# Kernel tuning notes

Measured on AMD Instinct MI355X. Metric: run time of the kernel, lower is better.

## Reference

```python
import jax, jax.numpy as jnp
import numpy as np

TEMPERATURE = 0.07


def _unit(k, shape):
    x = jax.random.normal(k, shape, dtype=jnp.float32)
    return x / jnp.linalg.norm(x, axis=-1, keepdims=True)


def setup_inputs() -> dict:
    key = jax.random.key(0)
    ks = jax.random.split(key, 7)
    B, Cml, Cmc, D = 8192, 2048, 1000, 512
    features = _unit(ks[0], (B, D))
    ml_text = _unit(ks[1], (Cml, D))
    mc_text = _unit(ks[2], (Cmc, D))
    multilabel_targets = (jax.random.uniform(ks[3], (B, Cml)) < 0.05).astype(jnp.float32)
    # one-hot multiclass targets
    mc_idx = jax.random.randint(ks[4], (B,), 0, Cmc)
    multiclass_targets = jax.nn.one_hot(mc_idx, Cmc, dtype=jnp.float32)
    dataset_indices = jax.random.randint(ks[5], (B,), 0, 2).astype(jnp.int32)
    ratios = jax.random.uniform(ks[6], (Cml,), minval=0.05, maxval=0.95, dtype=jnp.float32)
    return {
        "features": features,
        "multilabel_text_features": ml_text,
        "multiclass_text_features": mc_text,
        "multilabel_targets": multilabel_targets,
        "multiclass_targets": multiclass_targets,
        "dataset_indices": dataset_indices,
        "ratios": ratios,
    }


def iterate_M(sim_matrix, b, num_iterations=2):
    # sim_matrix: [B, C, 2]; b: [C, 2]
    P = jnp.exp(sim_matrix)
    for _ in range(num_iterations):
        P = P / P.sum(axis=2, keepdims=True)          # row (last-dim) normalize
        P = P / (P.sum(axis=0) / b)                   # column normalize to marginals b
    return P


def iterate_P(sim_matrix, m, num_iterations=5):
    # sim_matrix: [B, C]
    P = jnp.exp(sim_matrix)
    for _ in range(num_iterations):
        row_sums = P.sum(axis=1)
        P = P / jnp.maximum(row_sums, 1.0)[:, None]
        P = P * m / P.sum()
    return P


def reference(features, multilabel_text_features, multiclass_text_features,
              multilabel_targets, multiclass_targets, dataset_indices, ratios):
    ml_sim = features @ multilabel_text_features.T / TEMPERATURE   # [B, Cml]
    mc_sim = features @ multiclass_text_features.T / TEMPERATURE   # [B, Cmc]

    n_mc = jnp.sum(dataset_indices == 1).astype(jnp.float32)
    n_ml = jnp.sum(dataset_indices == 0).astype(jnp.float32)
    m = n_mc + n_ml * 0.1

    P = iterate_P(mc_sim, m, 5)

    bs = ml_sim.shape[0]
    sim3 = jnp.stack([ml_sim / 2, -ml_sim / 2], axis=-1)           # [B, Cml, 2]
    b = jnp.stack([ratios, 1.0 - ratios], axis=1) * bs             # [Cml, 2]
    M = iterate_M(sim3, b, 2)

    ml_targets_final = jnp.stack([multilabel_targets, 1.0 - multilabel_targets], axis=-1)
    multilabel_loss = -jnp.sum(ml_targets_final * jnp.log(M)) * 0.5
    multiclass_loss = -jnp.sum(multiclass_targets * jnp.log(P))
    total_loss = multiclass_loss + multilabel_loss
    return total_loss
```

## Files before the change

### kernel.cpp

```cpp
#include <hip/hip_runtime.h>

typedef unsigned short u16;
typedef float f32x4 __attribute__((ext_vector_type(4)));
typedef short s16x8 __attribute__((ext_vector_type(8)));

#define GPTR(x) ((const __attribute__((address_space(1))) void*)(x))
#define LPTR(x) ((__attribute__((address_space(3))) void*)(x))

__device__ __forceinline__ u16 f32_to_bf16(float f) {
  unsigned u = __builtin_bit_cast(unsigned, f);
  u += 0x7FFFu + ((u >> 16) & 1u);
  return (u16)(u >> 16);
}
__device__ __forceinline__ float bf16_to_f32(u16 h) {
  unsigned u = ((unsigned)h) << 16;
  return __builtin_bit_cast(float, u);
}

__global__ void k_cvt4(const float* __restrict__ in, u16* __restrict__ out, int n4) {
  int i = blockIdx.x * 256 + threadIdx.x;
  if (i >= n4) return;
  float4 v = reinterpret_cast<const float4*>(in)[i];
  ushort4 o;
  o.x = f32_to_bf16(v.x); o.y = f32_to_bf16(v.y);
  o.z = f32_to_bf16(v.z); o.w = f32_to_bf16(v.w);
  reinterpret_cast<ushort4*>(out)[i] = o;
}

__global__ void k_cvt_pad4(const float* __restrict__ in, u16* __restrict__ out, int nreal_rows) {
  int i = blockIdx.x * 256 + threadIdx.x;
  if (i >= 1024 * 128) return;
  int row = (i * 4) >> 9;
  ushort4 o = {0, 0, 0, 0};
  if (row < nreal_rows) {
    float4 v = reinterpret_cast<const float4*>(in)[i];
    o.x = f32_to_bf16(v.x); o.y = f32_to_bf16(v.y);
    o.z = f32_to_bf16(v.z); o.w = f32_to_bf16(v.w);
  }
  reinterpret_cast<ushort4*>(out)[i] = o;
}

template <bool COLSUM>
__global__ __launch_bounds__(256) void k_gemm_bt(
    const u16* __restrict__ A, const u16* __restrict__ B,
    u16* __restrict__ Cbf, float* __restrict__ colpart, int N, float scale)
{
  constexpr int K = 512;
  constexpr int BK = 64;
  __shared__ __align__(16) u16 As[128 * BK];
  __shared__ __align__(16) u16 Bs[128 * BK];
  const int tid  = threadIdx.x;
  const int lane = tid & 63;
  const int wave = tid >> 6;
  const int wr = wave >> 1, wc = wave & 1;
  const int row0 = blockIdx.x * 128;
  const int col0 = blockIdx.y * 128;

  f32x4 acc[4][4];
#pragma unroll
  for (int i = 0; i < 4; ++i)
#pragma unroll
    for (int j = 0; j < 4; ++j) acc[i][j] = (f32x4){0.f, 0.f, 0.f, 0.f};

  for (int k0 = 0; k0 < K; k0 += BK) {
    __syncthreads();
#pragma unroll
    for (int q = 0; q < 4; ++q) {
      int base = wave * 256 + q * 64;
      int slot = base + lane;
      int r = slot >> 3, s = slot & 7;
      int sg = s ^ (r & 7);
      __builtin_amdgcn_global_load_lds(GPTR(A + (size_t)(row0 + r) * K + k0 + sg * 8),
                                       LPTR(&As[base * 8]), 16, 0, 0);
      __builtin_amdgcn_global_load_lds(GPTR(B + (size_t)(col0 + r) * K + k0 + sg * 8),
                                       LPTR(&Bs[base * 8]), 16, 0, 0);
    }
    __syncthreads();
#pragma unroll
    for (int ks = 0; ks < 2; ++ks) {
      s16x8 af[4], bf[4];
#pragma unroll
      for (int mm = 0; mm < 4; ++mm) {
        int r = wr * 64 + mm * 16 + (lane & 15);
        int ss = (ks * 4 + (lane >> 4)) ^ (r & 7);
        af[mm] = *reinterpret_cast<const s16x8*>(&As[r * BK + ss * 8]);
      }
#pragma unroll
      for (int nn = 0; nn < 4; ++nn) {
        int r = wc * 64 + nn * 16 + (lane & 15);
        int ss = (ks * 4 + (lane >> 4)) ^ (r & 7);
        bf[nn] = *reinterpret_cast<const s16x8*>(&Bs[r * BK + ss * 8]);
      }
#pragma unroll
      for (int mm = 0; mm < 4; ++mm)
#pragma unroll
        for (int nn = 0; nn < 4; ++nn)
          acc[mm][nn] = __builtin_amdgcn_mfma_f32_16x16x32_bf16(af[mm], bf[nn], acc[mm][nn], 0, 0, 0);
    }
  }
  const int cr = (lane >> 4) * 4;
  const int cc = lane & 15;
#pragma unroll
  for (int mm = 0; mm < 4; ++mm) {
    int orow = row0 + wr * 64 + mm * 16 + cr;
#pragma unroll
    for (int nn = 0; nn < 4; ++nn) {
      int ocol = col0 + wc * 64 + nn * 16 + cc;
#pragma unroll
      for (int r = 0; r < 4; ++r)
        Cbf[(size_t)(orow + r) * N + ocol] = f32_to_bf16(acc[mm][nn][r] * scale);
    }
  }

  if constexpr (COLSUM) {
    __shared__ float cp[128];
    if (tid < 128) cp[tid] = 0.f;
    __syncthreads();
#pragma unroll
    for (int nn = 0; nn < 4; ++nn) {
      float cs = 0.f;
#pragma unroll
      for (int mm = 0; mm < 4; ++mm)
#pragma unroll
        for (int r = 0; r < 4; ++r) {
          float s = acc[mm][nn][r] * scale;
          cs += 1.f / (1.f + __expf(-s));
        }
      cs += __shfl_xor(cs, 16);
      cs += __shfl_xor(cs, 32);
      if (lane < 16) atomicAdd(&cp[wc * 64 + nn * 16 + lane], cs);
    }
    __syncthreads();
    if (tid < 128) colpart[(size_t)blockIdx.x * 2048 + col0 + tid] = cp[tid];
  }
}

__global__ void k_reduce_c(const float* __restrict__ part, const float* __restrict__ ratios,
                           float* __restrict__ c) {
  int j = blockIdx.x * 256 + threadIdx.x;
  float s = 0.f;
  for (int ch = 0; ch < 64; ++ch) s += part[ch * 2048 + j];
  float b0 = ratios[j] * 8192.f;
  float b1 = (1.f - ratios[j]) * 8192.f;
  c[2 * j]     = b0 / s;
  c[2 * j + 1] = b1 / (8192.f - s);
}

__global__ __launch_bounds__(256) void k_ml_pass2(
    const u16* __restrict__ S, const float* __restrict__ T, const float* __restrict__ c,
    float* __restrict__ part2, float* __restrict__ partT, float* __restrict__ partE)
{
  const int t = threadIdx.x;
  const int r0 = blockIdx.x * 8;
  float c0[8], c1[8];
#pragma unroll
  for (int q = 0; q < 4; ++q) {
    float4 cv = reinterpret_cast<const float4*>(c)[t * 4 + q];
    c0[q * 2]     = cv.x; c1[q * 2]     = cv.y;
    c0[q * 2 + 1] = cv.z; c1[q * 2 + 1] = cv.w;
  }

  float q0s[8], ts[8];
#pragma unroll
  for (int k = 0; k < 8; ++k) { q0s[k] = 0.f; ts[k] = 0.f; }
  float tss = 0.f, ldsum = 0.f;

#pragma unroll 2
  for (int r = 0; r < 8; ++r) {
    size_t row = r0 + r;
    s16x8 sv = *reinterpret_cast<const s16x8*>(S + row * 2048 + t * 8);
    float4 ta = reinterpret_cast<const float4*>(T + row * 2048)[t * 2];
    float4 tb = reinterpret_cast<const float4*>(T + row * 2048)[t * 2 + 1];
    float tv[8] = {ta.x, ta.y, ta.z, ta.w, tb.x, tb.y, tb.z, tb.w};
#pragma unroll
    for (int k = 0; k < 8; ++k) {
      float s = bf16_to_f32((u16)sv[k]);
      float e = __expf(s);
      float n0 = e * c0[k];
      float den = n0 + c1[k];
      q0s[k] += n0 * __builtin_amdgcn_rcpf(den);
      ldsum  += __logf(den);
      ts[k]  += tv[k];
      tss    += tv[k] * s;
    }
  }
  float es = tss - ldsum;
#pragma unroll
  for (int k = 0; k < 8; ++k)
    es += __logf(c0[k] / c1[k]) * ts[k] + 8.f * __logf(c1[k]);

  float* p2 = part2 + (size_t)blockIdx.x * 2048 + t * 8;
  float* pT = partT + (size_t)blockIdx.x * 2048 + t * 8;
#pragma unroll
  for (int q = 0; q < 2; ++q) {
    reinterpret_cast<float4*>(p2)[q] = (float4){q0s[q*4], q0s[q*4+1], q0s[q*4+2], q0s[q*4+3]};
    reinterpret_cast<float4*>(pT)[q] = (float4){ts[q*4], ts[q*4+1], ts[q*4+2], ts[q*4+3]};
  }

  __shared__ float red[256];
  red[t] = es;
  __syncthreads();
  for (int o = 128; o; o >>= 1) {
    if (t < o) red[t] += red[t + o];
    __syncthreads();
  }
  if (t == 0) partE[blockIdx.x] = red[0];
}

__global__ __launch_bounds__(256) void k_colredA(
    const float* __restrict__ part2, const float* __restrict__ partT,
    float* __restrict__ pA2, float* __restrict__ pAT)
{
  int j = blockIdx.x * 256 + threadIdx.x;
  int ch0 = blockIdx.y * 128;
  float cs2 = 0.f, Tj = 0.f;
  for (int ch = ch0; ch < ch0 + 128; ++ch) {
    cs2 += part2[(size_t)ch * 2048 + j];
    Tj  += partT[(size_t)ch * 2048 + j];
  }
  pA2[(size_t)blockIdx.y * 2048 + j] = cs2;
  pAT[(size_t)blockIdx.y * 2048 + j] = Tj;
}

__global__ __launch_bounds__(256) void k_colredB(
    const float* __restrict__ pA2, const float* __restrict__ pAT,
    const float* __restrict__ ratios, float* __restrict__ partCol)
{
  int j = blockIdx.x * 256 + threadIdx.x;
  float cs2 = 0.f, Tj = 0.f;
  for (int ch = 0; ch < 8; ++ch) {
    cs2 += pA2[(size_t)ch * 2048 + j];
    Tj  += pAT[(size_t)ch * 2048 + j];
  }
  float b0 = ratios[j] * 8192.f;
  float b1 = (1.f - ratios[j]) * 8192.f;
  float colp = Tj * __logf(b0 / cs2) + (8192.f - Tj) * __logf(b1 / (8192.f - cs2));
  __shared__ float red[256];
  red[threadIdx.x] = colp;
  __syncthreads();
  for (int o = 128; o; o >>= 1) {
    if (threadIdx.x < o) red[threadIdx.x] += red[threadIdx.x + o];
    __syncthreads();
  }
  if (threadIdx.x == 0) partCol[blockIdx.x] = red[0];
}

__global__ __launch_bounds__(256) void k_mc_rows(
    const u16* __restrict__ S2, const float* __restrict__ T2,
    float* __restrict__ R, float* __restrict__ rowdot, float* __restrict__ trow)
{
  int wave = threadIdx.x >> 6, lane = threadIdx.x & 63;
  int row = blockIdx.x * 4 + wave;
  const u16* s = S2 + (size_t)row * 1024;
  const float* t = T2 + (size_t)row * 1000;
  float re = 0.f, rd = 0.f, tr = 0.f;
#pragma unroll
  for (int g0 = 0; g0 < 2; ++g0) {
    int g = lane + g0 * 64;
    if (g < 125) {
      s16x8 sv = *reinterpret_cast<const s16x8*>(s + g * 8);
      float4 ta = reinterpret_cast<const float4*>(t)[g * 2];
      float4 tb = reinterpret_cast<const float4*>(t)[g * 2 + 1];
      float tv[8] = {ta.x, ta.y, ta.z, ta.w, tb.x, tb.y, tb.z, tb.w};
#pragma unroll
      for (int k = 0; k < 8; ++k) {
        float sf = bf16_to_f32((u16)sv[k]);
        re += __expf(sf);
        rd += tv[k] * sf;
        tr += tv[k];
      }
    }
  }
#pragma unroll
  for (int o = 32; o; o >>= 1) {
    re += __shfl_down(re, o);
    rd += __shfl_down(rd, o);
    tr += __shfl_down(tr, o);
  }
  if (lane == 0) { R[row] = re; rowdot[row] = rd; trow[row] = tr; }
}

__global__ __launch_bounds__(1024) void k_finalize(
    const float* __restrict__ R, const float* __restrict__ rowdot, const float* __restrict__ trow,
    const int* __restrict__ ds,
    const float* __restrict__ partE, const float* __restrict__ partCol,
    float* __restrict__ out)
{
  __shared__ float red[1024];
  const int tid = threadIdx.x;

  auto bsum = [&](float v) -> float {
    __syncthreads();
    red[tid] = v;
    __syncthreads();
    for (int o = 512; o; o >>= 1) {
      if (tid < o) red[tid] += red[tid + o];
      __syncthreads();
    }
    return red[0];
  };

  float nmc = 0.f, nml = 0.f;
  for (int i = tid; i < 8192; i += 1024) {
    int d = ds[i];
    nmc += (d == 1) ? 1.f : 0.f;
    nml += (d == 0) ? 1.f : 0.f;
  }
  float n_mc = bsum(nmc);
  float n_ml = bsum(nml);
  float m = n_mc + 0.1f * n_ml;

  float a[8], Rv[8];
#pragma unroll
  for (int q = 0; q < 8; ++q) { Rv[q] = R[tid + q * 1024]; a[q] = 1.f; }
  for (int it = 0; it < 5; ++it) {
    float p = 0.f;
#pragma unroll
    for (int q = 0; q < 8; ++q) {
      a[q] = a[q] / fmaxf(Rv[q] * a[q], 1.f);
      p += Rv[q] * a[q];
    }
    float tot = bsum(p);
    float sc = m / tot;
#pragma unroll
    for (int q = 0; q < 8; ++q) a[q] *= sc;
  }
  float mcp = 0.f;
#pragma unroll
  for (int q = 0; q < 8; ++q) {
    int i = tid + q * 1024;
    mcp += rowdot[i] + trow[i] * __logf(a[q]);
  }

  float ep = partE[tid];
  float cp = 0.f;
  if (tid < 8) cp = partCol[tid];

  float total = bsum(-mcp - 0.5f * (cp + ep));
  if (tid == 0) out[0] = total;
}

extern "C" void kernel_launch(void* const* d_in, const int* in_sizes, int n_in,
                              void* d_out, int out_size, void* d_ws, size_t ws_size,
                              hipStream_t stream)
{
  const float* features = (const float*)d_in[0];
  const float* ml_text  = (const float*)d_in[1];
  const float* mc_text  = (const float*)d_in[2];
  const float* ml_tgt   = (const float*)d_in[3];
  const float* mc_tgt   = (const float*)d_in[4];
  const int*   dsidx    = (const int*)d_in[5];
  const float* ratios   = (const float*)d_in[6];
  float* out = (float*)d_out;

  char* ws = (char*)d_ws;
  size_t off = 0;
  auto alloc = [&](size_t bytes) -> void* {
    void* p = ws + off;
    off += (bytes + 255) & ~(size_t)255;
    return p;
  };
  u16*   Abf    = (u16*)alloc((size_t)8192 * 512 * 2);
  u16*   MLbf   = (u16*)alloc((size_t)2048 * 512 * 2);
  u16*   MCbf   = (u16*)alloc((size_t)1024 * 512 * 2);
  u16*   Sml    = (u16*)alloc((size_t)8192 * 2048 * 2);
  u16*   Smc    = (u16*)alloc((size_t)8192 * 1024 * 2);
  float* part1  = (float*)alloc((size_t)64 * 2048 * 4);
  float* cbuf   = (float*)alloc((size_t)2048 * 2 * 4);
  float* part2  = (float*)alloc((size_t)1024 * 2048 * 4);
  float* partT  = (float*)alloc((size_t)1024 * 2048 * 4);
  float* pA2    = (float*)alloc((size_t)8 * 2048 * 4);
  float* pAT    = (float*)alloc((size_t)8 * 2048 * 4);
  float* partE  = (float*)alloc((size_t)1024 * 4);
  float* partCol= (float*)alloc((size_t)8 * 4);
  float* Rbuf   = (float*)alloc((size_t)8192 * 4);
  float* rdot   = (float*)alloc((size_t)8192 * 4);
  float* trow   = (float*)alloc((size_t)8192 * 4);

  k_cvt4<<<(8192 * 128 + 255) / 256, 256, 0, stream>>>(features, Abf, 8192 * 128);
  k_cvt4<<<(2048 * 128 + 255) / 256, 256, 0, stream>>>(ml_text, MLbf, 2048 * 128);
  k_cvt_pad4<<<(1024 * 128 + 255) / 256, 256, 0, stream>>>(mc_text, MCbf, 1000);

  const float scale = 1.0f / 0.07f;
  k_gemm_bt<true ><<<dim3(64, 16), 256, 0, stream>>>(Abf, MLbf, Sml, part1, 2048, scale);
  k_gemm_bt<false><<<dim3(64, 8),  256, 0, stream>>>(Abf, MCbf, Smc, nullptr, 1024, scale);

  k_reduce_c<<<8, 256, 0, stream>>>(part1, ratios, cbuf);
  k_ml_pass2<<<1024, 256, 0, stream>>>(Sml, ml_tgt, cbuf, part2, partT, partE);
  k_mc_rows<<<2048, 256, 0, stream>>>(Smc, mc_tgt, Rbuf, rdot, trow);
  k_colredA<<<dim3(8, 8), 256, 0, stream>>>(part2, partT, pA2, pAT);
  k_colredB<<<8, 256, 0, stream>>>(pA2, pAT, ratios, partCol);
  k_finalize<<<1, 1024, 0, stream>>>(Rbuf, rdot, trow, dsidx, partE, partCol, out);
}
```

Measured before the change: 130.7 us.

## Fuse multiclass row reductions into GEMM epilogue and merge conversion kernels

Result: slower. 143.4 us (+9.7%).

```diff
diff --git a/kernel.cpp b/kernel.cpp
--- a/kernel.cpp
+++ b/kernel.cpp
@@ -17,33 +17,35 @@
   return __builtin_bit_cast(float, u);
 }
 
-__global__ void k_cvt4(const float* __restrict__ in, u16* __restrict__ out, int n4) {
+__global__ __launch_bounds__(256) void k_cvt_all(
+    const float* __restrict__ A, const float* __restrict__ ML, const float* __restrict__ MC,
+    u16* __restrict__ Abf, u16* __restrict__ MLbf, u16* __restrict__ MCbf)
+{
   int i = blockIdx.x * 256 + threadIdx.x;
-  if (i >= n4) return;
-  float4 v = reinterpret_cast<const float4*>(in)[i];
-  ushort4 o;
-  o.x = f32_to_bf16(v.x); o.y = f32_to_bf16(v.y);
-  o.z = f32_to_bf16(v.z); o.w = f32_to_bf16(v.w);
-  reinterpret_cast<ushort4*>(out)[i] = o;
-}
-
-__global__ void k_cvt_pad4(const float* __restrict__ in, u16* __restrict__ out, int nreal_rows) {
-  int i = blockIdx.x * 256 + threadIdx.x;
-  if (i >= 1024 * 128) return;
-  int row = (i * 4) >> 9;
+  const float* src; u16* dst; int idx;
+  bool pad = false;
+  if (i < 1048576) { src = A; dst = Abf; idx = i; }
+  else if (i < 1310720) { src = ML; dst = MLbf; idx = i - 1048576; }
+  else if (i < 1441792) {
+    idx = i - 1310720; src = MC; dst = MCbf;
+    pad = ((idx * 4) >> 9) >= 1000;
+  } else return;
   ushort4 o = {0, 0, 0, 0};
-  if (row < nreal_rows) {
-    float4 v = reinterpret_cast<const float4*>(in)[i];
+  if (!pad) {
+    float4 v = reinterpret_cast<const float4*>(src)[idx];
     o.x = f32_to_bf16(v.x); o.y = f32_to_bf16(v.y);
     o.z = f32_to_bf16(v.z); o.w = f32_to_bf16(v.w);
   }
-  reinterpret_cast<ushort4*>(out)[i] = o;
-}
-
-template <bool COLSUM>
+  reinterpret_cast<ushort4*>(dst)[idx] = o;
+}
+
+template <int MODE>
 __global__ __launch_bounds__(256) void k_gemm_bt(
     const u16* __restrict__ A, const u16* __restrict__ B,
-    u16* __restrict__ Cbf, float* __restrict__ colpart, int N, float scale)
+    u16* __restrict__ Cbf, float* __restrict__ colpart,
+    const float* __restrict__ T2, float* __restrict__ pexp,
+    float* __restrict__ prdt, float* __restrict__ ptrw,
+    int N, float scale)
 {
   constexpr int K = 512;
   constexpr int BK = 64;
@@ -55,6 +57,8 @@
   const int wr = wave >> 1, wc = wave & 1;
   const int row0 = blockIdx.x * 128;
   const int col0 = blockIdx.y * 128;
+  const int cr = (lane >> 4) * 4;
+  const int cc = lane & 15;
 
   f32x4 acc[4][4];
 #pragma unroll
@@ -98,21 +102,19 @@
           acc[mm][nn] = __builtin_amdgcn_mfma_f32_16x16x32_bf16(af[mm], bf[nn], acc[mm][nn], 0, 0, 0);
     }
   }
-  const int cr = (lane >> 4) * 4;
-  const int cc = lane & 15;
-#pragma unroll
-  for (int mm = 0; mm < 4; ++mm) {
-    int orow = row0 + wr * 64 + mm * 16 + cr;
-#pragma unroll
-    for (int nn = 0; nn < 4; ++nn) {
-      int ocol = col0 + wc * 64 + nn * 16 + cc;
-#pragma unroll
-      for (int r = 0; r < 4; ++r)
-        Cbf[(size_t)(orow + r) * N + ocol] = f32_to_bf16(acc[mm][nn][r] * scale);
-    }
-  }
-
-  if constexpr (COLSUM) {
+
+  if constexpr (MODE == 0) {
+#pragma unroll
+    for (int mm = 0; mm < 4; ++mm) {
+      int orow = row0 + wr * 64 + mm * 16 + cr;
+#pragma unroll
+      for (int nn = 0; nn < 4; ++nn) {
+        int ocol = col0 + wc * 64 + nn * 16 + cc;
+#pragma unroll
+        for (int r = 0; r < 4; ++r)
+          Cbf[(size_t)(orow + r) * N + ocol] = f32_to_bf16(acc[mm][nn][r] * scale);
+      }
+    }
     __shared__ float cp[128];
     if (tid < 128) cp[tid] = 0.f;
     __syncthreads();
@@ -132,6 +134,56 @@
     }
     __syncthreads();
     if (tid < 128) colpart[(size_t)blockIdx.x * 2048 + col0 + tid] = cp[tid];
+  }
+
+  if constexpr (MODE == 1) {
+    float ex[16], rd[16], tw[16];
+#pragma unroll
+    for (int mm = 0; mm < 4; ++mm)
+#pragma unroll
+      for (int r = 0; r < 4; ++r) {
+        float e = 0.f, d = 0.f, w = 0.f;
+        int row = row0 + wr * 64 + mm * 16 + cr + r;
+#pragma unroll
+        for (int nn = 0; nn < 4; ++nn) {
+          int ocol = col0 + wc * 64 + nn * 16 + cc;
+          float s = acc[mm][nn][r] * scale;
+          if (ocol < 1000) {
+            float t = T2[(size_t)row * 1000 + ocol];
+            e += __expf(s);
+            d += t * s;
+            w += t;
+          }
+        }
+        ex[mm * 4 + r] = e; rd[mm * 4 + r] = d; tw[mm * 4 + r] = w;
+      }
+#pragma unroll
+    for (int o = 1; o < 16; o <<= 1)
+#pragma unroll
+      for (int q = 0; q < 16; ++q) {
+        ex[q] += __shfl_xor(ex[q], o);
+        rd[q] += __shfl_xor(rd[q], o);
+        tw[q] += __shfl_xor(tw[q], o);
+      }
+    __shared__ float rex[128][2], rrd[128][2], rtw[128][2];
+    if ((lane & 15) == 0) {
+#pragma unroll
+      for (int mm = 0; mm < 4; ++mm)
+#pragma unroll
+        for (int r = 0; r < 4; ++r) {
+          int lrow = wr * 64 + mm * 16 + cr + r;
+          rex[lrow][wc] = ex[mm * 4 + r];
+          rrd[lrow][wc] = rd[mm * 4 + r];
+          rtw[lrow][wc] = tw[mm * 4 + r];
+        }
+    }
+    __syncthreads();
+    if (tid < 128) {
+      size_t o = (size_t)blockIdx.y * 8192 + row0 + tid;
+      pexp[o] = rex[tid][0] + rex[tid][1];
+      prdt[o] = rrd[tid][0] + rrd[tid][1];
+      ptrw[o] = rtw[tid][0] + rtw[tid][1];
+    }
   }
 }
 
@@ -212,9 +264,9 @@
     float* __restrict__ pA2, float* __restrict__ pAT)
 {
   int j = blockIdx.x * 256 + threadIdx.x;
-  int ch0 = blockIdx.y * 128;
+  int ch0 = blockIdx.y * 16;
   float cs2 = 0.f, Tj = 0.f;
-  for (int ch = ch0; ch < ch0 + 128; ++ch) {
+  for (int ch = ch0; ch < ch0 + 16; ++ch) {
     cs2 += part2[(size_t)ch * 2048 + j];
     Tj  += partT[(size_t)ch * 2048 + j];
   }
@@ -228,7 +280,7 @@
 {
   int j = blockIdx.x * 256 + threadIdx.x;
   float cs2 = 0.f, Tj = 0.f;
-  for (int ch = 0; ch < 8; ++ch) {
+  for (int ch = 0; ch < 64; ++ch) {
     cs2 += pA2[(size_t)ch * 2048 + j];
     Tj  += pAT[(size_t)ch * 2048 + j];
   }
@@ -245,43 +297,8 @@
   if (threadIdx.x == 0) partCol[blockIdx.x] = red[0];
 }
 
-__global__ __launch_bounds__(256) void k_mc_rows(
-    const u16* __restrict__ S2, const float* __restrict__ T2,
-    float* __restrict__ R, float* __restrict__ rowdot, float* __restrict__ trow)
-{
-  int wave = threadIdx.x >> 6, lane = threadIdx.x & 63;
-  int row = blockIdx.x * 4 + wave;
-  const u16* s = S2 + (size_t)row * 1024;
-  const float* t = T2 + (size_t)row * 1000;
-  float re = 0.f, rd = 0.f, tr = 0.f;
-#pragma unroll
-  for (int g0 = 0; g0 < 2; ++g0) {
-    int g = lane + g0 * 64;
-    if (g < 125) {
-      s16x8 sv = *reinterpret_cast<const s16x8*>(s + g * 8);
-      float4 ta = reinterpret_cast<const float4*>(t)[g * 2];
-      float4 tb = reinterpret_cast<const float4*>(t)[g * 2 + 1];
-      float tv[8] = {ta.x, ta.y, ta.z, ta.w, tb.x, tb.y, tb.z, tb.w};
-#pragma unroll
-      for (int k = 0; k < 8; ++k) {
-        float sf = bf16_to_f32((u16)sv[k]);
-        re += __expf(sf);
-        rd += tv[k] * sf;
-        tr += tv[k];
-      }
-    }
-  }
-#pragma unroll
-  for (int o = 32; o; o >>= 1) {
-    re += __shfl_down(re, o);
-    rd += __shfl_down(rd, o);
-    tr += __shfl_down(tr, o);
-  }
-  if (lane == 0) { R[row] = re; rowdot[row] = rd; trow[row] = tr; }
-}
-
 __global__ __launch_bounds__(1024) void k_finalize(
-    const float* __restrict__ R, const float* __restrict__ rowdot, const float* __restrict__ trow,
+    const float* __restrict__ pexp, const float* __restrict__ prdt, const float* __restrict__ ptrw,
     const int* __restrict__ ds,
     const float* __restrict__ partE, const float* __restrict__ partCol,
     float* __restrict__ out)
@@ -310,9 +327,19 @@
   float n_ml = bsum(nml);
   float m = n_mc + 0.1f * n_ml;
 
-  float a[8], Rv[8];
-#pragma unroll
-  for (int q = 0; q < 8; ++q) { Rv[q] = R[tid + q * 1024]; a[q] = 1.f; }
+  float a[8], Rv[8], rdv[8], twv[8];
+#pragma unroll
+  for (int q = 0; q < 8; ++q) {
+    int i = tid + q * 1024;
+    float e = 0.f, d = 0.f, w = 0.f;
+#pragma unroll
+    for (int ch = 0; ch < 8; ++ch) {
+      e += pexp[(size_t)ch * 8192 + i];
+      d += prdt[(size_t)ch * 8192 + i];
+      w += ptrw[(size_t)ch * 8192 + i];
+    }
+    Rv[q] = e; rdv[q] = d; twv[q] = w; a[q] = 1.f;
+  }
   for (int it = 0; it < 5; ++it) {
     float p = 0.f;
 #pragma unroll
@@ -327,10 +354,8 @@
   }
   float mcp = 0.f;
 #pragma unroll
-  for (int q = 0; q < 8; ++q) {
-    int i = tid + q * 1024;
-    mcp += rowdot[i] + trow[i] * __logf(a[q]);
-  }
+  for (int q = 0; q < 8; ++q)
+    mcp += rdv[q] + twv[q] * __logf(a[q]);
 
   float ep = partE[tid];
   float cp = 0.f;
@@ -364,31 +389,29 @@
   u16*   MLbf   = (u16*)alloc((size_t)2048 * 512 * 2);
   u16*   MCbf   = (u16*)alloc((size_t)1024 * 512 * 2);
   u16*   Sml    = (u16*)alloc((size_t)8192 * 2048 * 2);
-  u16*   Smc    = (u16*)alloc((size_t)8192 * 1024 * 2);
   float* part1  = (float*)alloc((size_t)64 * 2048 * 4);
   float* cbuf   = (float*)alloc((size_t)2048 * 2 * 4);
   float* part2  = (float*)alloc((size_t)1024 * 2048 * 4);
   float* partT  = (float*)alloc((size_t)1024 * 2048 * 4);
-  float* pA2    = (float*)alloc((size_t)8 * 2048 * 4);
-  float* pAT    = (float*)alloc((size_t)8 * 2048 * 4);
+  float* pA2    = (float*)alloc((size_t)64 * 2048 * 4);
+  float* pAT    = (float*)alloc((size_t)64 * 2048 * 4);
   float* partE  = (float*)alloc((size_t)1024 * 4);
   float* partCol= (float*)alloc((size_t)8 * 4);
-  float* Rbuf   = (float*)alloc((size_t)8192 * 4);
-  float* rdot   = (float*)alloc((size_t)8192 * 4);
-  float* trow   = (float*)alloc((size_t)8192 * 4);
-
-  k_cvt4<<<(8192 * 128 + 255) / 256, 256, 0, stream>>>(features, Abf, 8192 * 128);
-  k_cvt4<<<(2048 * 128 + 255) / 256, 256, 0, stream>>>(ml_text, MLbf, 2048 * 128);
-  k_cvt_pad4<<<(1024 * 128 + 255) / 256, 256, 0, stream>>>(mc_text, MCbf, 1000);
+  float* pexp   = (float*)alloc((size_t)8 * 8192 * 4);
+  float* prdt   = (float*)alloc((size_t)8 * 8192 * 4);
+  float* ptrw   = (float*)alloc((size_t)8 * 8192 * 4);
+
+  k_cvt_all<<<(1441792 + 255) / 256, 256, 0, stream>>>(features, ml_text, mc_text, Abf, MLbf, MCbf);
 
   const float scale = 1.0f / 0.07f;
-  k_gemm_bt<true ><<<dim3(64, 16), 256, 0, stream>>>(Abf, MLbf, Sml, part1, 2048, scale);
-  k_gemm_bt<false><<<dim3(64, 8),  256, 0, stream>>>(Abf, MCbf, Smc, nullptr, 1024, scale);
+  k_gemm_bt<0><<<dim3(64, 16), 256, 0, stream>>>(Abf, MLbf, Sml, part1,
+                                                 nullptr, nullptr, nullptr, nullptr, 2048, scale);
+  k_gemm_bt<1><<<dim3(64, 8),  256, 0, stream>>>(Abf, MCbf, nullptr, nullptr,
+                                                 mc_tgt, pexp, prdt, ptrw, 1024, scale);
 
   k_reduce_c<<<8, 256, 0, stream>>>(part1, ratios, cbuf);
   k_ml_pass2<<<1024, 256, 0, stream>>>(Sml, ml_tgt, cbuf, part2, partT, partE);
-  k_mc_rows<<<2048, 256, 0, stream>>>(Smc, mc_tgt, Rbuf, rdot, trow);
-  k_colredA<<<dim3(8, 8), 256, 0, stream>>>(part2, partT, pA2, pAT);
+  k_colredA<<<dim3(8, 64), 256, 0, stream>>>(part2, partT, pA2, pAT);
   k_colredB<<<8, 256, 0, stream>>>(pA2, pAT, ratios, partCol);
-  k_finalize<<<1, 1024, 0, stream>>>(Rbuf, rdot, trow, dsidx, partE, partCol, out);
-}
+  k_finalize<<<1, 1024, 0, stream>>>(pexp, prdt, ptrw, dsidx, partE, partCol, out);
+}
```
